# Kernel tuning notes

Hardware: AMD Instinct MI355X
Metric: run time of the kernel (lower is better)

The kernel has to match this reference:

```python
import jax, jax.numpy as jnp
import numpy as np

N_BUS = 2000
BATCH = 512
N_EDGES = 3072000
SN_MVA = 100.0
ALPHA = 0.9
PHYS_SCALE = 0.02
DEG2RAD = np.pi / 180.0


def setup_inputs() -> dict:
    key = jax.random.key(0)
    ks = jax.random.split(key, 13)
    N = BATCH * N_BUS
    return {
        "y_pred": jax.random.normal(ks[0], (BATCH, N_BUS * 2), jnp.float32),
        "y_true": jax.random.normal(ks[1], (BATCH, N_BUS * 2), jnp.float32),
        "x_input": jax.random.normal(ks[2], (N, 7), jnp.float32),
        "edge_index": jax.random.randint(ks[3], (2, N_EDGES), 0, N),
        "edge_attr": jax.random.normal(ks[4], (N_EDGES, 4), jnp.float32),
        "x_mean": jax.random.normal(ks[5], (N_BUS, 7), jnp.float32),
        "x_std": jax.random.uniform(ks[6], (N_BUS, 7), jnp.float32, 0.5, 1.5),
        "y_mean": jax.random.normal(ks[7], (N_BUS, 2), jnp.float32),
        "y_std": jax.random.uniform(ks[8], (N_BUS, 2), jnp.float32, 0.5, 1.5),
        "edge_mean": jax.random.normal(ks[9], (4,), jnp.float32),
        "edge_std": jax.random.uniform(ks[10], (4,), jnp.float32, 0.5, 1.5),
        "load_bus_mask": jax.random.bernoulli(ks[11], 0.8, (N_BUS,)),
        "bus_shunt_pu": jax.random.normal(ks[12], (N_BUS, 2), jnp.float32) * 0.01,
    }


def reference(y_pred, y_true, x_input, edge_index, edge_attr,
              x_mean, x_std, y_mean, y_std, edge_mean, edge_std,
              load_bus_mask, bus_shunt_pu):
    B, n = BATCH, N_BUS
    N = B * n
    # --- MSE in denormalised target space ---
    yp = y_pred.reshape(B, n, 2) * y_std + y_mean   # [B, n, 2] (Vm, Va_deg)
    yt = y_true.reshape(B, n, 2) * y_std + y_mean
    mse = jnp.mean((yp - yt) ** 2)
    # --- denormalise node features ---
    x_pq = (x_input.reshape(B, n, 7)[:, :, :2] * x_std[:, :2] + x_mean[:, :2])
    x_pq = x_pq.reshape(N, 2) / SN_MVA              # per-unit P, Q demand
    x_phys = jnp.concatenate([yp.reshape(N, 2), x_pq], axis=-1)  # [N,4] Vm,Va,P,Q
    edge_pu = edge_attr * edge_std + edge_mean      # [E,4] Gs,Bs,Gm,Bm
    # --- per-edge power-flow message (flow='target_to_source': i=row0, j=row1) ---
    src, dst = edge_index[0], edge_index[1]
    xi = x_phys[src]
    xj = x_phys[dst]
    vm_i, va_i = xi[:, 0], xi[:, 1] * DEG2RAD
    vm_j, va_j = xj[:, 0], xj[:, 1] * DEG2RAD
    e_i, f_i = vm_i * jnp.cos(va_i), vm_i * jnp.sin(va_i)
    e_j, f_j = vm_j * jnp.cos(va_j), vm_j * jnp.sin(va_j)
    Gs, Bs, Gm, Bm = edge_pu[:, 0], edge_pu[:, 1], edge_pu[:, 2], edge_pu[:, 3]
    I_re = Gs * e_i - Bs * f_i + Gm * e_j - Bm * f_j
    I_im = Gs * f_i + Bs * e_i + Gm * f_j + Bm * e_j
    Pji = -(e_i * I_re + f_i * I_im)
    Qji = -(f_i * I_re - e_i * I_im)
    msg = jnp.stack([Pji, Qji], axis=-1)            # [E,2]
    # --- scatter-add aggregation into source nodes ---
    agg = jax.ops.segment_sum(msg, src, num_segments=N)  # [N,2]
    # --- KCL residual per node ---
    vm_sq = x_phys[:, 0] ** 2
    shunt = jnp.tile(bus_shunt_pu, (B, 1))          # [N,2]
    dP = -agg[:, 0] + x_phys[:, 2] + vm_sq * shunt[:, 0]
    dQ = -agg[:, 1] + x_phys[:, 3] - vm_sq * shunt[:, 1]
    sq = dP ** 2 + dQ ** 2                          # [N]
    w = jnp.tile(load_bus_mask, B).astype(sq.dtype)
    phys = jnp.sum(sq * w) / jnp.sum(w)             # masked mean
    return ALPHA * mse + (1.0 - ALPHA) * PHYS_SCALE * phys
```

## Files before the change

### kernel.cpp

```cpp
#include <hip/hip_runtime.h>
#include <hip/hip_bf16.h>
#include <hip/hip_fp16.h>

#define N_BUS   2000
#define BATCH   512
#define NNODES  (BATCH * N_BUS)
#define NEDGES  3072000

constexpr float SN_INV     = 0.01f;
constexpr float ALPHA_C    = 0.9f;
constexpr float PHYS_SCALE = 0.02f;
constexpr float DEG2RAD_C  = 0.017453292519943295f;

typedef float v4f __attribute__((ext_vector_type(4)));

__device__ __forceinline__ void atomic_pk_add_h2(__half2* addr, float P, float Q) {
    __half2 v = __floats2half2_rn(P, Q);
#if __has_builtin(__builtin_amdgcn_global_atomic_fadd_v2f16)
    typedef _Float16 v2h __attribute__((ext_vector_type(2)));
    __builtin_amdgcn_global_atomic_fadd_v2f16(
        (__attribute__((address_space(1))) v2h*)(void*)addr,
        *reinterpret_cast<v2h*>(&v));
#else
    unsafeAtomicAdd(addr, v);
#endif
}

__device__ __forceinline__ float wave_reduce(float v) {
    #pragma unroll
    for (int off = 32; off > 0; off >>= 1) v += __shfl_down(v, off, 64);
    return v;
}

__global__ __launch_bounds__(256) void node_prep(
    const float* __restrict__ y_pred, const float* __restrict__ y_true,
    const float* __restrict__ y_mean, const float* __restrict__ y_std,
    __half2* __restrict__ ef, __half2* __restrict__ agg, float* __restrict__ acc)
{
    int t = blockIdx.x * blockDim.x + threadIdx.x;
    int n0 = t * 4;
    int i0 = n0 % N_BUS;
    float4 pr0 = reinterpret_cast<const float4*>(y_pred + (size_t)n0*2)[0];
    float4 pr1 = reinterpret_cast<const float4*>(y_pred + (size_t)n0*2)[1];
    float4 tr0 = reinterpret_cast<const float4*>(y_true + (size_t)n0*2)[0];
    float4 tr1 = reinterpret_cast<const float4*>(y_true + (size_t)n0*2)[1];
    float4 ys0 = reinterpret_cast<const float4*>(y_std  + (size_t)i0*2)[0];
    float4 ys1 = reinterpret_cast<const float4*>(y_std  + (size_t)i0*2)[1];
    float4 ym0 = reinterpret_cast<const float4*>(y_mean + (size_t)i0*2)[0];
    float4 ym1 = reinterpret_cast<const float4*>(y_mean + (size_t)i0*2)[1];

    float d, msep = 0.0f;
    d = (pr0.x - tr0.x) * ys0.x; msep = fmaf(d, d, msep);
    d = (pr0.y - tr0.y) * ys0.y; msep = fmaf(d, d, msep);
    d = (pr0.z - tr0.z) * ys0.z; msep = fmaf(d, d, msep);
    d = (pr0.w - tr0.w) * ys0.w; msep = fmaf(d, d, msep);
    d = (pr1.x - tr1.x) * ys1.x; msep = fmaf(d, d, msep);
    d = (pr1.y - tr1.y) * ys1.y; msep = fmaf(d, d, msep);
    d = (pr1.z - tr1.z) * ys1.z; msep = fmaf(d, d, msep);
    d = (pr1.w - tr1.w) * ys1.w; msep = fmaf(d, d, msep);

    float vmA = fmaf(pr0.x, ys0.x, ym0.x), vaA = fmaf(pr0.y, ys0.y, ym0.y);
    float vmB = fmaf(pr0.z, ys0.z, ym0.z), vaB = fmaf(pr0.w, ys0.w, ym0.w);
    float vmC = fmaf(pr1.x, ys1.x, ym1.x), vaC = fmaf(pr1.y, ys1.y, ym1.y);
    float vmD = fmaf(pr1.z, ys1.z, ym1.z), vaD = fmaf(pr1.w, ys1.w, ym1.w);
    float s, c;
    __sincosf(vaA * DEG2RAD_C, &s, &c); __half2 eA = __floats2half2_rn(vmA*c, vmA*s);
    __sincosf(vaB * DEG2RAD_C, &s, &c); __half2 eB = __floats2half2_rn(vmB*c, vmB*s);
    __sincosf(vaC * DEG2RAD_C, &s, &c); __half2 eC = __floats2half2_rn(vmC*c, vmC*s);
    __sincosf(vaD * DEG2RAD_C, &s, &c); __half2 eD = __floats2half2_rn(vmD*c, vmD*s);
    *reinterpret_cast<uint4*>(ef + n0) = make_uint4(
        *reinterpret_cast<unsigned*>(&eA), *reinterpret_cast<unsigned*>(&eB),
        *reinterpret_cast<unsigned*>(&eC), *reinterpret_cast<unsigned*>(&eD));
    *reinterpret_cast<uint4*>(agg + n0) = make_uint4(0u, 0u, 0u, 0u);

    __shared__ float red[4];
    float v = wave_reduce(msep);
    int lane = threadIdx.x & 63, wid = threadIdx.x >> 6;
    if (lane == 0) red[wid] = v;
    __syncthreads();
    if (threadIdx.x == 0)
        unsafeAtomicAdd(acc + 0, red[0] + red[1] + red[2] + red[3]);
}

__global__ __launch_bounds__(256) void edge_kernel(
    const int* __restrict__ eidx, const float* __restrict__ eattr,
    const float* __restrict__ e_mean, const float* __restrict__ e_std,
    const __half2* __restrict__ ef, __half2* __restrict__ agg)
{
    int e = blockIdx.x * blockDim.x + threadIdx.x;
    int s = __builtin_nontemporal_load(eidx + e);
    int d = __builtin_nontemporal_load(eidx + NEDGES + e);
    const v4f* eav = reinterpret_cast<const v4f*>(eattr) + e;
    v4f ea = __builtin_nontemporal_load(eav);
    float Gs = fmaf(ea.x, e_std[0], e_mean[0]);
    float Bs = fmaf(ea.y, e_std[1], e_mean[1]);
    float Gm = fmaf(ea.z, e_std[2], e_mean[2]);
    float Bm = fmaf(ea.w, e_std[3], e_mean[3]);
    float2 fi = __half22float2(ef[s]);
    float2 fj = __half22float2(ef[d]);
    float e_i = fi.x, f_i = fi.y;
    float e_j = fj.x, f_j = fj.y;
    float I_re = Gs*e_i - Bs*f_i + Gm*e_j - Bm*f_j;
    float I_im = Gs*f_i + Bs*e_i + Gm*f_j + Bm*e_j;
    float Pji = -(e_i*I_re + f_i*I_im);
    float Qji = -(f_i*I_re - e_i*I_im);
    atomic_pk_add_h2(agg + s, Pji, Qji);
}

__device__ __forceinline__ void node_term(
    unsigned efb, unsigned agb, float shP, float shQ, int m, long n, int i,
    const float* __restrict__ x_input, const float* __restrict__ x_mean,
    const float* __restrict__ x_std, float& sqw, float& wsum)
{
    float2 efk = __half22float2(*reinterpret_cast<__half2*>(&efb));
    float2 agk = __half22float2(*reinterpret_cast<__half2*>(&agb));
    float vm2 = fmaf(efk.x, efk.x, efk.y * efk.y);
    float p = fmaf(x_input[n*7 + 0], x_std[i*7 + 0], x_mean[i*7 + 0]) * SN_INV;
    float q = fmaf(x_input[n*7 + 1], x_std[i*7 + 1], x_mean[i*7 + 1]) * SN_INV;
    float dP = fmaf(vm2, shP, p) - agk.x;
    float dQ = fmaf(-vm2, shQ, q) - agk.y;
    float w = m ? 1.0f : 0.0f;
    sqw = fmaf(dP*dP + dQ*dQ, w, sqw);
    wsum += w;
}

__global__ __launch_bounds__(256) void node_final(
    const float* __restrict__ x_input,
    const float* __restrict__ x_mean, const float* __restrict__ x_std,
    const float* __restrict__ shunt, const int* __restrict__ mask,
    const __half2* __restrict__ ef, const __half2* __restrict__ agg,
    float* __restrict__ acc, float* __restrict__ out)
{
    int t = blockIdx.x * blockDim.x + threadIdx.x;
    int n0 = t * 4;
    int i0 = n0 % N_BUS;
    uint4 efu = *reinterpret_cast<const uint4*>(ef + n0);
    uint4 agu = *reinterpret_cast<const uint4*>(agg + n0);
    float4 sh0 = reinterpret_cast<const float4*>(shunt + (size_t)i0*2)[0];
    float4 sh1 = reinterpret_cast<const float4*>(shunt + (size_t)i0*2)[1];
    int4  mk  = *reinterpret_cast<const int4*>(mask + i0);

    float sqw = 0.0f, wsum = 0.0f;
    node_term(efu.x, agu.x, sh0.x, sh0.y, mk.x, (long)n0+0, i0+0, x_input, x_mean, x_std, sqw, wsum);
    node_term(efu.y, agu.y, sh0.z, sh0.w, mk.y, (long)n0+1, i0+1, x_input, x_mean, x_std, sqw, wsum);
    node_term(efu.z, agu.z, sh1.x, sh1.y, mk.z, (long)n0+2, i0+2, x_input, x_mean, x_std, sqw, wsum);
    node_term(efu.w, agu.w, sh1.z, sh1.w, mk.w, (long)n0+3, i0+3, x_input, x_mean, x_std, sqw, wsum);

    __shared__ float red0[4], red1[4];
    float v0 = wave_reduce(sqw);
    float v1 = wave_reduce(wsum);
    int lane = threadIdx.x & 63, wid = threadIdx.x >> 6;
    if (lane == 0) { red0[wid] = v0; red1[wid] = v1; }
    __syncthreads();
    if (threadIdx.x == 0) {
        unsafeAtomicAdd(acc + 1, red0[0] + red0[1] + red0[2] + red0[3]);
        unsafeAtomicAdd(acc + 2, red1[0] + red1[1] + red1[2] + red1[3]);
        __threadfence();
        unsigned prev = atomicAdd(reinterpret_cast<unsigned*>(acc + 3), 1u);
        if (prev == gridDim.x - 1) {
            float mse = unsafeAtomicAdd(acc + 0, 0.0f) * (1.0f / (2.0f * NNODES));
            float sq  = unsafeAtomicAdd(acc + 1, 0.0f);
            float ww  = unsafeAtomicAdd(acc + 2, 0.0f);
            out[0] = ALPHA_C * mse + (1.0f - ALPHA_C) * PHYS_SCALE * (sq / ww);
        }
    }
}

extern "C" void kernel_launch(void* const* d_in, const int* in_sizes, int n_in,
                              void* d_out, int out_size, void* d_ws, size_t ws_size,
                              hipStream_t stream) {
    const float* y_pred    = (const float*)d_in[0];
    const float* y_true    = (const float*)d_in[1];
    const float* x_input   = (const float*)d_in[2];
    const int*   edge_idx  = (const int*)  d_in[3];
    const float* edge_attr = (const float*)d_in[4];
    const float* x_mean    = (const float*)d_in[5];
    const float* x_std     = (const float*)d_in[6];
    const float* y_mean    = (const float*)d_in[7];
    const float* y_std     = (const float*)d_in[8];
    const float* edge_mean = (const float*)d_in[9];
    const float* edge_std  = (const float*)d_in[10];
    const int*   load_mask = (const int*)  d_in[11];
    const float* shunt     = (const float*)d_in[12];

    __half2* agg = (__half2*)d_ws;
    __half2* ef  = agg + NNODES;
    float*   acc = (float*)(ef + NNODES);

    (void)hipMemsetAsync(acc, 0, 16, stream);

    dim3 blk(256);
    node_prep<<<dim3(NNODES / 1024), blk, 0, stream>>>(
        y_pred, y_true, y_mean, y_std, ef, agg, acc);
    edge_kernel<<<dim3(NEDGES / 256), blk, 0, stream>>>(
        edge_idx, edge_attr, edge_mean, edge_std, ef, agg);
    node_final<<<dim3(NNODES / 1024), blk, 0, stream>>>(
        x_input, x_mean, x_std, shunt, load_mask, ef, agg, acc, (float*)d_out);
}
```

Before: 357.1 us.

## Privatize scatter-add accumulators per XCD to keep atomics in local L2

Each XCD now scatters into its own copy of the half2 aggregation buffer, picked by reading the hardware XCC id, so atomics stay in that die's L2 and avoid cross-die coherence traffic. The final node kernel sums the eight partial copies. Zeroing moves from node_prep to a large memset of all eight copies, and the atomic becomes an inline-asm global_atomic_pk_add_f16. The cost is eight times the accumulator memory (about 32 MB), extra memset bandwidth and eight reads per node in the final pass.

```diff
diff --git a/kernel.cpp b/kernel.cpp
--- a/kernel.cpp
+++ b/kernel.cpp
@@ -6,6 +6,7 @@
 #define BATCH   512
 #define NNODES  (BATCH * N_BUS)
 #define NEDGES  3072000
+#define NXCD    8
 
 constexpr float SN_INV     = 0.01f;
 constexpr float ALPHA_C    = 0.9f;
@@ -14,16 +15,17 @@
 
 typedef float v4f __attribute__((ext_vector_type(4)));
 
-__device__ __forceinline__ void atomic_pk_add_h2(__half2* addr, float P, float Q) {
+__device__ __forceinline__ void atomic_pk_add_h2_l2(__half2* addr, float P, float Q) {
     __half2 v = __floats2half2_rn(P, Q);
-#if __has_builtin(__builtin_amdgcn_global_atomic_fadd_v2f16)
-    typedef _Float16 v2h __attribute__((ext_vector_type(2)));
-    __builtin_amdgcn_global_atomic_fadd_v2f16(
-        (__attribute__((address_space(1))) v2h*)(void*)addr,
-        *reinterpret_cast<v2h*>(&v));
-#else
-    unsafeAtomicAdd(addr, v);
-#endif
+    unsigned u = *reinterpret_cast<unsigned*>(&v);
+    asm volatile("global_atomic_pk_add_f16 %0, %1, off"
+                 :: "v"(addr), "v"(u) : "memory");
+}
+
+__device__ __forceinline__ unsigned xcc_id() {
+    unsigned x;
+    asm("s_getreg_b32 %0, hwreg(HW_REG_XCC_ID)" : "=s"(x));
+    return x & (NXCD - 1);
 }
 
 __device__ __forceinline__ float wave_reduce(float v) {
@@ -35,7 +37,7 @@
 __global__ __launch_bounds__(256) void node_prep(
     const float* __restrict__ y_pred, const float* __restrict__ y_true,
     const float* __restrict__ y_mean, const float* __restrict__ y_std,
-    __half2* __restrict__ ef, __half2* __restrict__ agg, float* __restrict__ acc)
+    __half2* __restrict__ ef, float* __restrict__ acc)
 {
     int t = blockIdx.x * blockDim.x + threadIdx.x;
     int n0 = t * 4;
@@ -71,7 +73,6 @@
     *reinterpret_cast<uint4*>(ef + n0) = make_uint4(
         *reinterpret_cast<unsigned*>(&eA), *reinterpret_cast<unsigned*>(&eB),
         *reinterpret_cast<unsigned*>(&eC), *reinterpret_cast<unsigned*>(&eD));
-    *reinterpret_cast<uint4*>(agg + n0) = make_uint4(0u, 0u, 0u, 0u);
 
     __shared__ float red[4];
     float v = wave_reduce(msep);
@@ -85,8 +86,9 @@
 __global__ __launch_bounds__(256) void edge_kernel(
     const int* __restrict__ eidx, const float* __restrict__ eattr,
     const float* __restrict__ e_mean, const float* __restrict__ e_std,
-    const __half2* __restrict__ ef, __half2* __restrict__ agg)
-{
+    const __half2* __restrict__ ef, __half2* __restrict__ agg8)
+{
+    __half2* myagg = agg8 + (size_t)xcc_id() * NNODES;
     int e = blockIdx.x * blockDim.x + threadIdx.x;
     int s = __builtin_nontemporal_load(eidx + e);
     int d = __builtin_nontemporal_load(eidx + NEDGES + e);
@@ -104,21 +106,20 @@
     float I_im = Gs*f_i + Bs*e_i + Gm*f_j + Bm*e_j;
     float Pji = -(e_i*I_re + f_i*I_im);
     float Qji = -(f_i*I_re - e_i*I_im);
-    atomic_pk_add_h2(agg + s, Pji, Qji);
+    atomic_pk_add_h2_l2(myagg + s, Pji, Qji);
 }
 
 __device__ __forceinline__ void node_term(
-    unsigned efb, unsigned agb, float shP, float shQ, int m, long n, int i,
+    unsigned efb, float agx, float agy, float shP, float shQ, int m, long n, int i,
     const float* __restrict__ x_input, const float* __restrict__ x_mean,
     const float* __restrict__ x_std, float& sqw, float& wsum)
 {
     float2 efk = __half22float2(*reinterpret_cast<__half2*>(&efb));
-    float2 agk = __half22float2(*reinterpret_cast<__half2*>(&agb));
     float vm2 = fmaf(efk.x, efk.x, efk.y * efk.y);
     float p = fmaf(x_input[n*7 + 0], x_std[i*7 + 0], x_mean[i*7 + 0]) * SN_INV;
     float q = fmaf(x_input[n*7 + 1], x_std[i*7 + 1], x_mean[i*7 + 1]) * SN_INV;
-    float dP = fmaf(vm2, shP, p) - agk.x;
-    float dQ = fmaf(-vm2, shQ, q) - agk.y;
+    float dP = fmaf(vm2, shP, p) - agx;
+    float dQ = fmaf(-vm2, shQ, q) - agy;
     float w = m ? 1.0f : 0.0f;
     sqw = fmaf(dP*dP + dQ*dQ, w, sqw);
     wsum += w;
@@ -128,23 +129,37 @@
     const float* __restrict__ x_input,
     const float* __restrict__ x_mean, const float* __restrict__ x_std,
     const float* __restrict__ shunt, const int* __restrict__ mask,
-    const __half2* __restrict__ ef, const __half2* __restrict__ agg,
+    const __half2* __restrict__ ef, const __half2* __restrict__ agg8,
     float* __restrict__ acc, float* __restrict__ out)
 {
     int t = blockIdx.x * blockDim.x + threadIdx.x;
     int n0 = t * 4;
     int i0 = n0 % N_BUS;
     uint4 efu = *reinterpret_cast<const uint4*>(ef + n0);
-    uint4 agu = *reinterpret_cast<const uint4*>(agg + n0);
+
+    float agx[4] = {0,0,0,0}, agy[4] = {0,0,0,0};
+    #pragma unroll
+    for (int k = 0; k < NXCD; ++k) {
+        uint4 a = *reinterpret_cast<const uint4*>(agg8 + (size_t)k * NNODES + n0);
+        float2 a0 = __half22float2(*reinterpret_cast<__half2*>(&a.x));
+        float2 a1 = __half22float2(*reinterpret_cast<__half2*>(&a.y));
+        float2 a2 = __half22float2(*reinterpret_cast<__half2*>(&a.z));
+        float2 a3 = __half22float2(*reinterpret_cast<__half2*>(&a.w));
+        agx[0] += a0.x; agy[0] += a0.y;
+        agx[1] += a1.x; agy[1] += a1.y;
+        agx[2] += a2.x; agy[2] += a2.y;
+        agx[3] += a3.x; agy[3] += a3.y;
+    }
+
     float4 sh0 = reinterpret_cast<const float4*>(shunt + (size_t)i0*2)[0];
     float4 sh1 = reinterpret_cast<const float4*>(shunt + (size_t)i0*2)[1];
     int4  mk  = *reinterpret_cast<const int4*>(mask + i0);
 
     float sqw = 0.0f, wsum = 0.0f;
-    node_term(efu.x, agu.x, sh0.x, sh0.y, mk.x, (long)n0+0, i0+0, x_input, x_mean, x_std, sqw, wsum);
-    node_term(efu.y, agu.y, sh0.z, sh0.w, mk.y, (long)n0+1, i0+1, x_input, x_mean, x_std, sqw, wsum);
-    node_term(efu.z, agu.z, sh1.x, sh1.y, mk.z, (long)n0+2, i0+2, x_input, x_mean, x_std, sqw, wsum);
-    node_term(efu.w, agu.w, sh1.z, sh1.w, mk.w, (long)n0+3, i0+3, x_input, x_mean, x_std, sqw, wsum);
+    node_term(efu.x, agx[0], agy[0], sh0.x, sh0.y, mk.x, (long)n0+0, i0+0, x_input, x_mean, x_std, sqw, wsum);
+    node_term(efu.y, agx[1], agy[1], sh0.z, sh0.w, mk.y, (long)n0+1, i0+1, x_input, x_mean, x_std, sqw, wsum);
+    node_term(efu.z, agx[2], agy[2], sh1.x, sh1.y, mk.z, (long)n0+2, i0+2, x_input, x_mean, x_std, sqw, wsum);
+    node_term(efu.w, agx[3], agy[3], sh1.z, sh1.w, mk.w, (long)n0+3, i0+3, x_input, x_mean, x_std, sqw, wsum);
 
     __shared__ float red0[4], red1[4];
     float v0 = wave_reduce(sqw);
@@ -183,17 +198,18 @@
     const int*   load_mask = (const int*)  d_in[11];
     const float* shunt     = (const float*)d_in[12];
 
-    __half2* agg = (__half2*)d_ws;
-    __half2* ef  = agg + NNODES;
-    float*   acc = (float*)(ef + NNODES);
-
+    __half2* agg8 = (__half2*)d_ws;
+    __half2* ef   = agg8 + (size_t)NXCD * NNODES;
+    float*   acc  = (float*)(ef + NNODES);
+
+    (void)hipMemsetAsync(agg8, 0, (size_t)NXCD * NNODES * sizeof(__half2), stream);
     (void)hipMemsetAsync(acc, 0, 16, stream);
 
     dim3 blk(256);
     node_prep<<<dim3(NNODES / 1024), blk, 0, stream>>>(
-        y_pred, y_true, y_mean, y_std, ef, agg, acc);
+        y_pred, y_true, y_mean, y_std, ef, acc);
     edge_kernel<<<dim3(NEDGES / 256), blk, 0, stream>>>(
-        edge_idx, edge_attr, edge_mean, edge_std, ef, agg);
+        edge_idx, edge_attr, edge_mean, edge_std, ef, agg8);
     node_final<<<dim3(NNODES / 1024), blk, 0, stream>>>(
-        x_input, x_mean, x_std, shunt, load_mask, ef, agg, acc, (float*)d_out);
-}
+        x_input, x_mean, x_std, shunt, load_mask, ef, agg8, acc, (float*)d_out);
+}
```

Measured after the change: 371.3 us. 1.04x slower.
